# Performance work log

Measured on AMD Instinct MI355X. Metric: run time of the kernel, lower is better.

Reference implementation:

```python
import jax, jax.numpy as jnp
import numpy as np

B, T, N, F_IN = 8, 12, 20000, 2
H, HORIZON, K = 64, 12, 2
E = 320000


def setup_inputs() -> dict:
    key = jax.random.key(0)
    ks = jax.random.split(key, 12)
    s = 0.05
    return dict(
        x=jax.random.normal(ks[0], (B, T, N, F_IN), jnp.float32),
        edge_index=jax.random.randint(ks[1], (2, E), 0, N),
        edge_weight=jax.random.uniform(ks[2], (E,), jnp.float32),
        enc_w=jax.random.normal(ks[3], (F_IN, H), jnp.float32) * s,
        enc_b=jnp.zeros((H,), jnp.float32),
        node_emb=jax.random.normal(ks[4], (N, H), jnp.float32) * s,
        w_ih=jax.random.normal(ks[5], (3 * H, H), jnp.float32) * s,
        w_hh=jax.random.normal(ks[6], (3 * H, H), jnp.float32) * s,
        b_ih=jnp.zeros((3 * H,), jnp.float32),
        b_hh=jnp.zeros((3 * H,), jnp.float32),
        filt_w=jax.random.normal(ks[7], (H * (2 * K + 1), H), jnp.float32) * s,
        filt_b=jnp.zeros((H,), jnp.float32),
        dec_w=jax.random.normal(ks[8], (H, F_IN * HORIZON), jnp.float32) * s,
        dec_b=jnp.zeros((F_IN * HORIZON,), jnp.float32),
    )


def _gru_last(x_seq, w_ih, w_hh, b_ih, b_hh):
    # x_seq: [BN, T, H] -> last hidden state [BN, H] (torch GRU gate math)
    bn = x_seq.shape[0]
    h0 = jnp.zeros((bn, H), x_seq.dtype)
    # precompute input-side gates: [T, BN, 3H]
    xg = jnp.swapaxes(jnp.einsum('bth,gh->btg', x_seq, w_ih) + b_ih, 0, 1)

    def step(h, xg_t):
        hg = h @ w_hh.T + b_hh
        xr, xz, xn = jnp.split(xg_t, 3, axis=-1)
        hr, hz, hn = jnp.split(hg, 3, axis=-1)
        r = jax.nn.sigmoid(xr + hr)
        z = jax.nn.sigmoid(xz + hz)
        n = jnp.tanh(xn + r * hn)
        return (1.0 - z) * n + z * h, None

    h_last, _ = jax.lax.scan(step, h0, xg)
    return h_last


def _norm_weights(w, idx):
    # normalize edge weights by in-degree of aggregation index (tsl normalize)
    deg = jax.ops.segment_sum(w, idx, num_segments=N)
    inv = jnp.where(deg > 0, 1.0 / deg, 0.0)
    return w * inv[idx]


def _propagate(h, src, tgt, w):
    # h: [B, N, H]; message x_j * w aggregated (sum) at target
    msg = h[:, src, :] * w[None, :, None]           # [B, E, H]
    return jnp.zeros_like(h).at[:, tgt, :].add(msg)


def reference(x, edge_index, edge_weight, enc_w, enc_b, node_emb,
              w_ih, w_hh, b_ih, b_hh, filt_w, filt_b, dec_w, dec_b):
    b, t, n, _ = x.shape
    # linear encode + node embeddings
    x_emb = x @ enc_w + enc_b + node_emb[None, None]          # [B, T, N, H]
    # per-node GRU over time
    x_rnn = jnp.transpose(x_emb, (0, 2, 1, 3)).reshape(b * n, t, H)
    h = _gru_last(x_rnn, w_ih, w_hh, b_ih, b_hh).reshape(b, n, H)
    # diffusion graph conv: root + k hops forward + k hops backward
    src, tgt = edge_index[0], edge_index[1]
    w_fwd = _norm_weights(edge_weight, tgt)
    w_bwd = _norm_weights(edge_weight, src)
    outs = [h]
    for s_idx, t_idx, w in ((src, tgt, w_fwd), (tgt, src, w_bwd)):
        hs = h
        for _ in range(K):
            hs = _propagate(hs, s_idx, t_idx, w)
            outs.append(hs)
    z = jnp.concatenate(outs, axis=-1) @ filt_w + filt_b      # [B, N, H]
    # decode and rearrange 'b n (t f) -> b t n f'
    x_out = z @ dec_w + dec_b                                 # [B, N, HORIZON*F_IN]
    x_hor = x_out.reshape(b, n, HORIZON, F_IN)
    return jnp.transpose(x_hor, (0, 2, 1, 3))                 # [B, HORIZON, N, F_IN]
```

## Files before the change

kernel.cpp:

```cpp
#include <hip/hip_runtime.h>

#define NN 20000
#define NE 320000
#define NB 8
#define NT 12

typedef unsigned int u32;
typedef short bf16x8 __attribute__((ext_vector_type(8)));
typedef float f32x4 __attribute__((ext_vector_type(4)));
typedef u32   u32x2 __attribute__((ext_vector_type(2)));

union U8 { u32 u[4]; bf16x8 v; };

__device__ __forceinline__ float bcast(float v, int k) {
  return __int_as_float(__builtin_amdgcn_readlane(__float_as_int(v), k));
}
__device__ __forceinline__ u32 cvt_pk_bf16(float a, float b) {
  u32 r;
  asm("v_cvt_pk_bf16_f32 %0, %1, %2" : "=v"(r) : "v"(a), "v"(b));
  return r;
}
__device__ __forceinline__ float rcpf(float x) {
  float r;
  asm("v_rcp_f32 %0, %1" : "=v"(r) : "v"(x));
  return r;
}
__device__ __forceinline__ unsigned short f2bf(float f) {
  u32 u = __float_as_uint(f);
  u32 r = (u + 0x7FFFu + ((u >> 16) & 1u)) >> 16;
  return (unsigned short)r;
}
__device__ __forceinline__ float bf2f(unsigned short s) {
  return __uint_as_float(((u32)s) << 16);
}

__global__ void deg_kernel(const int* __restrict__ ei, const float* __restrict__ ew,
                           float* __restrict__ wsum_f, float* __restrict__ wsum_b,
                           int* __restrict__ cnt_f, int* __restrict__ cnt_b) {
  int e = blockIdx.x * 256 + threadIdx.x;
  if (e >= NE) return;
  int s = ei[e], t = ei[NE + e];
  float wv = ew[e];
  atomicAdd(&wsum_f[t], wv);
  atomicAdd(&cnt_f[t], 1);
  atomicAdd(&wsum_b[s], wv);
  atomicAdd(&cnt_b[s], 1);
}

__global__ __launch_bounds__(1024) void scan_kernel(
    const int* __restrict__ cnt_f, const int* __restrict__ cnt_b,
    int* __restrict__ rp_f, int* __restrict__ rp_b,
    int* __restrict__ cur_f, int* __restrict__ cur_b) {
  __shared__ int sm[1024];
  const int tid = threadIdx.x;
  for (int pass = 0; pass < 2; ++pass) {
    const int* cnt = pass ? cnt_b : cnt_f;
    int* rp  = pass ? rp_b  : rp_f;
    int* cur = pass ? cur_b : cur_f;
    const int base = tid * 20;
    int4 c4[5];
    int s = 0;
    if (base < NN) {
      const int4* cp = (const int4*)(cnt + base);
#pragma unroll
      for (int j = 0; j < 5; j++) c4[j] = cp[j];
#pragma unroll
      for (int j = 0; j < 5; j++) s += c4[j].x + c4[j].y + c4[j].z + c4[j].w;
    }
    __syncthreads();
    sm[tid] = s;
    __syncthreads();
    for (int off = 1; off < 1024; off <<= 1) {
      int v = (tid >= off) ? sm[tid - off] : 0;
      __syncthreads();
      sm[tid] += v;
      __syncthreads();
    }
    if (base < NN) {
      int run = sm[tid] - s;
      int4* rp4  = (int4*)(rp + base);
      int4* cur4 = (int4*)(cur + base);
#pragma unroll
      for (int j = 0; j < 5; j++) {
        int4 o;
        o.x = run; run += c4[j].x;
        o.y = run; run += c4[j].y;
        o.z = run; run += c4[j].z;
        o.w = run; run += c4[j].w;
        rp4[j] = o;
        cur4[j] = o;
      }
    }
    if (tid == 1023) rp[NN] = sm[1023];
  }
}

__global__ void fill_kernel(const int* __restrict__ ei, const float* __restrict__ ew,
                            const float* __restrict__ wsum_f, const float* __restrict__ wsum_b,
                            int* __restrict__ cur_f, int* __restrict__ cur_b,
                            int* __restrict__ col_f, float* __restrict__ wn_f,
                            int* __restrict__ col_b, float* __restrict__ wn_b) {
  int e = blockIdx.x * 256 + threadIdx.x;
  if (e >= NE) return;
  int s = ei[e], t = ei[NE + e];
  float wv = ew[e];
  int slot = atomicAdd(&cur_f[t], 1);
  float w1 = wsum_f[t];
  col_f[slot] = s;
  wn_f[slot] = (w1 > 0.f) ? wv / w1 : 0.f;
  slot = atomicAdd(&cur_b[s], 1);
  float w2 = wsum_b[s];
  col_b[slot] = t;
  wn_b[slot] = (w2 > 0.f) ? wv / w2 : 0.f;
}

#define NBLK_NB 313
__global__ __launch_bounds__(512) void nb_kernel(
    const float* __restrict__ node_emb, const float* __restrict__ enc_b,
    const float* __restrict__ w_ih, const float* __restrict__ b_ih,
    const float* __restrict__ enc_w, const float* __restrict__ b_hh,
    const float* __restrict__ filt_w, const float* __restrict__ filt_b,
    const float* __restrict__ dec_w, const float* __restrict__ dec_b,
    float* __restrict__ nbq, float* __restrict__ W2,
    float* __restrict__ Wcat, float* __restrict__ cbv) {
  const int tid = threadIdx.x;
  if (blockIdx.x >= NBLK_NB) {
    int idx = (blockIdx.x - NBLK_NB) * 512 + tid;
    if (idx < 64 * 128) {
      int k = idx >> 7, j = idx & 127;
      float acc = 0.f;
      if (j < 120) {
        int wi = j / 24, jj = j - wi * 24;
        for (int c = 0; c < 64; c++)
          acc += filt_w[(wi * 64 + k) * 64 + c] * dec_w[c * 24 + jj];
      }
      Wcat[idx] = acc;
    } else if (idx < 64 * 128 + 24) {
      int jj = idx - 64 * 128;
      float acc = dec_b[jj];
      for (int c = 0; c < 64; c++) acc += filt_b[c] * dec_w[c * 24 + jj];
      cbv[jj] = acc;
    }
    return;
  }
  __shared__ float w3[64 * 64 * 4];
  for (int idx = tid; idx < 192 * 64; idx += 512) {
    int row = idx >> 6, k = idx & 63;
    w3[((k << 6) + (row & 63)) * 4 + (row >> 6)] = w_ih[idx];
  }
  __syncthreads();
  const int lane = tid & 63, wave = tid >> 6;
  const float4* w3v = (const float4*)w3;
  const float eb = enc_b[lane];
  const float bir = b_ih[lane], biz = b_ih[64 + lane], bin_ = b_ih[128 + lane];
  const float bhr = b_hh[lane], bhz = b_hh[64 + lane];
#pragma unroll 1
  for (int pass = 0; pass < 8; ++pass) {
    const int n = blockIdx.x * 64 + pass * 8 + wave;
    if (n >= NN) break;
    float ne = node_emb[n * 64 + lane] + eb;
    float ar = bir, az = biz, an = bin_;
#pragma unroll 16
    for (int k = 0; k < 64; k++) {
      float4 w = w3v[(k << 6) + lane];
      float nk = bcast(ne, k);
      ar = fmaf(w.x, nk, ar);
      az = fmaf(w.y, nk, az);
      an = fmaf(w.z, nk, an);
    }
    nbq[(((lane >> 2)) * NN + n) * 4 + (lane & 3)]      = ar + bhr;
    nbq[((16 + (lane >> 2)) * NN + n) * 4 + (lane & 3)] = az + bhz;
    nbq[((32 + (lane >> 2)) * NN + n) * 4 + (lane & 3)] = an;
  }
  if (blockIdx.x == 0 && tid < 384) {
    int f = tid / 192, g = tid - f * 192;
    float acc = 0.f;
    for (int k2 = 0; k2 < 64; k2++) acc += enc_w[f * 64 + k2] * w_ih[g * 64 + k2];
    W2[f * 192 + g] = acc;
  }
}

#define MFMA(acc, a, b) acc = __builtin_amdgcn_mfma_f32_16x16x32_bf16((a), (b), acc, 0, 0, 0)

__global__ __launch_bounds__(256) void gru_kernel(
    const float* __restrict__ x, const float* __restrict__ nbq,
    const float* __restrict__ W2, const float* __restrict__ b_hh,
    const float* __restrict__ w_hh, const float* __restrict__ Wcat,
    const float* __restrict__ cbv,
    float* __restrict__ G0, float* __restrict__ G1f, float* __restrict__ G2f,
    float* __restrict__ G1b, float* __restrict__ G2b) {
  __shared__ u32 lds[16384];
  const int tid = threadIdx.x;

  for (int e = tid; e < 6144; e += 256) {
    int gate = e >> 5, k2 = (e & 31) << 1;
    float w0 = w_hh[gate * 64 + k2];
    float w1 = w_hh[gate * 64 + k2 + 1];
    unsigned short h0 = f2bf(w0), h1 = f2bf(w1);
    unsigned short l0 = f2bf(w0 - bf2f(h0)), l1 = f2bf(w1 - bf2f(h1));
    int tile = gate >> 4, ks = k2 >> 5;
    int ln = (gate & 15) + (((k2 >> 3) & 3) << 4);
    int r = (k2 >> 1) & 3;
    int idx = ((tile * 2 + ks) << 8) + (ln << 2) + r;
    lds[idx]        = (u32)h0 | ((u32)h1 << 16);
    lds[6144 + idx] = (u32)l0 | ((u32)l1 << 16);
  }
  __syncthreads();

  const int lane = tid & 63, wave = tid >> 6;
  const int g = lane >> 4, sl = lane & 15;
  const int seq = blockIdx.x * 64 + wave * 16 + sl;
  const int bb = seq / NN;
  const int node = seq - bb * NN;
  const u32 hxbase = 12288 + wave * 1024;
  const u32 xsw = ((u32)(sl & 3)) << 2;

  u32 w2h[12], w2l[12];
#pragma unroll
  for (int tl = 0; tl < 12; tl++) {
    float w0 = W2[tl * 16 + sl], w1 = W2[192 + tl * 16 + sl];
    u32 ph = cvt_pk_bf16(w0, w1);
    float lo0 = w0 - __uint_as_float(ph << 16);
    float lo1 = w1 - __uint_as_float(ph & 0xffff0000u);
    u32 pl = cvt_pk_bf16(lo0, lo1);
    w2h[tl] = (lane < 16) ? ph : 0u;
    w2l[tl] = (lane < 16) ? pl : 0u;
  }

  f32x4 nbA[4], nbB[4], nbC[4], bhnv[4];
#pragma unroll
  for (int fb = 0; fb < 4; fb++) {
    nbA[fb]  = *(const f32x4*)(nbq + ((size_t)(fb * 4 + g) * NN + node) * 4);
    nbB[fb]  = *(const f32x4*)(nbq + ((size_t)(16 + fb * 4 + g) * NN + node) * 4);
    nbC[fb]  = *(const f32x4*)(nbq + ((size_t)(32 + fb * 4 + g) * NN + node) * 4);
    bhnv[fb] = *(const f32x4*)(b_hh + 128 + fb * 16 + g * 4);
  }

  f32x4 hreg[4];
#pragma unroll
  for (int fb = 0; fb < 4; fb++) hreg[fb] = (f32x4){0.f, 0.f, 0.f, 0.f};

  const float* xptr = x + ((size_t)(bb * NT) * NN + node) * 2;

#define LDW(tile, ks, part) (*(const bf16x8*)(lds + (part) * 6144 + (((tile) * 2 + (ks)) << 8) + (lane << 2)))
#define RDX(q) (*(const bf16x8*)(lds + hxbase + (q) * 256 + sl * 16 + (((u32)(g * 4)) ^ xsw)))

  bf16x8 hb0, hb1, lb0, lb1;

  float2 xv = *(const float2*)(xptr);

#pragma unroll 1
  for (int t = 0; t < NT; t++) {
    float2 xvn;
    if (t + 1 < NT) xvn = *(const float2*)(xptr + (size_t)(t + 1) * (NN * 2));
    u32 xhw = cvt_pk_bf16(xv.x, xv.y);
    float xl0 = xv.x - __uint_as_float(xhw << 16);
    float xl1 = xv.y - __uint_as_float(xhw & 0xffff0000u);
    u32 xlw = cvt_pk_bf16(xl0, xl1);
    U8 xB;
    xB.u[0] = xhw; xB.u[1] = xlw; xB.u[2] = xhw; xB.u[3] = 0u;

    if (t) { hb0 = RDX(0); hb1 = RDX(1); lb0 = RDX(2); lb1 = RDX(3); }

#pragma unroll
    for (int fb = 0; fb < 4; fb++) {
      f32x4 aR = nbA[fb], aZ = nbB[fb], aXN = nbC[fb], aHN = bhnv[fb];
      if (t) {
        bf16x8 Ah0 = LDW(fb, 0, 0), Al0 = LDW(fb, 0, 1);
        bf16x8 Ah1 = LDW(fb, 1, 0), Al1 = LDW(fb, 1, 1);
        MFMA(aR, Ah0, hb0); MFMA(aR, Ah0, lb0); MFMA(aR, Al0, hb0);
        MFMA(aR, Ah1, hb1); MFMA(aR, Ah1, lb1); MFMA(aR, Al1, hb1);
        bf16x8 Bh0 = LDW(4 + fb, 0, 0), Bl0 = LDW(4 + fb, 0, 1);
        bf16x8 Bh1 = LDW(4 + fb, 1, 0), Bl1 = LDW(4 + fb, 1, 1);
        MFMA(aZ, Bh0, hb0); MFMA(aZ, Bh0, lb0); MFMA(aZ, Bl0, hb0);
        MFMA(aZ, Bh1, hb1); MFMA(aZ, Bh1, lb1); MFMA(aZ, Bl1, hb1);
        bf16x8 Ch0 = LDW(8 + fb, 0, 0), Cl0 = LDW(8 + fb, 0, 1);
        bf16x8 Ch1 = LDW(8 + fb, 1, 0), Cl1 = LDW(8 + fb, 1, 1);
        MFMA(aHN, Ch0, hb0); MFMA(aHN, Ch0, lb0); MFMA(aHN, Cl0, hb0);
        MFMA(aHN, Ch1, hb1); MFMA(aHN, Ch1, lb1); MFMA(aHN, Cl1, hb1);
      }
      U8 aW;
      aW.u[0] = w2h[fb];     aW.u[1] = w2h[fb];     aW.u[2] = w2l[fb];     aW.u[3] = 0u;
      MFMA(aR, aW.v, xB.v);
      aW.u[0] = w2h[4 + fb]; aW.u[1] = w2h[4 + fb]; aW.u[2] = w2l[4 + fb];
      MFMA(aZ, aW.v, xB.v);
      aW.u[0] = w2h[8 + fb]; aW.u[1] = w2h[8 + fb]; aW.u[2] = w2l[8 + fb];
      MFMA(aXN, aW.v, xB.v);

      float hv[4];
#pragma unroll
      for (int r = 0; r < 4; r++) {
        float rr = rcpf(1.f + __expf(-aR[r]));
        float zz = rcpf(1.f + __expf(-aZ[r]));
        float nv = fmaf(rr, aHN[r], aXN[r]);
        float th = fmaf(-2.f, rcpf(1.f + __expf(2.f * nv)), 1.f);
        float h2 = fmaf(zz, hreg[fb][r] - th, th);
        hreg[fb][r] = h2;
        hv[r] = h2;
      }
      u32 hiA = cvt_pk_bf16(hv[0], hv[1]);
      u32 hiB = cvt_pk_bf16(hv[2], hv[3]);
      float l0 = hv[0] - __uint_as_float(hiA << 16);
      float l1 = hv[1] - __uint_as_float(hiA & 0xffff0000u);
      float l2 = hv[2] - __uint_as_float(hiB << 16);
      float l3 = hv[3] - __uint_as_float(hiB & 0xffff0000u);
      u32 loA = cvt_pk_bf16(l0, l1);
      u32 loB = cvt_pk_bf16(l2, l3);
      u32 wo = hxbase + ((u32)(fb >> 1)) * 256 + sl * 16 + (((u32)((fb & 1) * 8 + g * 2)) ^ xsw);
      *(u32x2*)(lds + wo)       = (u32x2){hiA, hiB};
      *(u32x2*)(lds + wo + 512) = (u32x2){loA, loB};
    }
    xv = xvn;
  }

  __syncthreads();
  for (int e = tid; e < 4096; e += 256) {
    int j = e >> 5, k2 = (e & 31) << 1;
    float w0 = Wcat[k2 * 128 + j];
    float w1 = Wcat[(k2 + 1) * 128 + j];
    unsigned short h0 = f2bf(w0), h1 = f2bf(w1);
    unsigned short l0 = f2bf(w0 - bf2f(h0)), l1 = f2bf(w1 - bf2f(h1));
    int tile = j >> 4, ks = k2 >> 5;
    int ln = (j & 15) + (((k2 >> 3) & 3) << 4);
    int r = (k2 >> 1) & 3;
    int idx = ((tile * 2 + ks) << 8) + (ln << 2) + r;
    lds[idx]        = (u32)h0 | ((u32)h1 << 16);
    lds[4096 + idx] = (u32)l0 | ((u32)l1 << 16);
  }
  __syncthreads();
  hb0 = RDX(0); hb1 = RDX(1); lb0 = RDX(2); lb1 = RDX(3);

#define LDC(tile, ks, part) (*(const bf16x8*)(lds + (part) * 4096 + (((tile) * 2 + (ks)) << 8) + (lane << 2)))
#pragma unroll
  for (int tile = 0; tile < 8; tile++) {
    f32x4 acc = (f32x4){0.f, 0.f, 0.f, 0.f};
    bf16x8 Ah0 = LDC(tile, 0, 0), Al0 = LDC(tile, 0, 1);
    MFMA(acc, Ah0, hb0); MFMA(acc, Ah0, lb0); MFMA(acc, Al0, hb0);
    bf16x8 Ah1 = LDC(tile, 1, 0), Al1 = LDC(tile, 1, 1);
    MFMA(acc, Ah1, hb1); MFMA(acc, Ah1, lb1); MFMA(acc, Al1, hb1);
#pragma unroll
    for (int r = 0; r < 4; r++) {
      int j = tile * 16 + g * 4 + r;
      if (j < 120) {
        int wi = j / 24, jj = j - wi * 24;
        float val = acc[r];
        if (wi == 0) val += cbv[jj];
        float* gb = (wi == 0) ? G0 : (wi == 1) ? G1f : (wi == 2) ? G2f : (wi == 3) ? G1b : G2b;
        gb[((size_t)node * NB + bb) * 24 + jj] = val;
      }
    }
  }
}

__global__ __launch_bounds__(256) void hop1_kernel(
    float* __restrict__ G1f, const float* __restrict__ G2f,
    float* __restrict__ G1b, const float* __restrict__ G2b,
    const int* __restrict__ rp_f, const int* __restrict__ col_f, const float* __restrict__ wn_f,
    const int* __restrict__ rp_b, const int* __restrict__ col_b, const float* __restrict__ wn_b) {
  const int wv = threadIdx.x >> 6;
  const int lane = threadIdx.x & 63;
  const int task = blockIdx.x * 4 + wv;
  const int fwd = task < NN;
  const int n = fwd ? task : task - NN;
  const int* rp  = fwd ? rp_f : rp_b;
  const int* col = fwd ? col_f : col_b;
  const float* wn = fwd ? wn_f : wn_b;
  const float4* src = (const float4*)(fwd ? G2f : G2b);
  float4* dst = (float4*)(fwd ? G1f : G1b);
  const int e0 = rp[n], e1 = rp[n + 1];
  if (lane >= 48) return;
  float4 acc = {0.f, 0.f, 0.f, 0.f};
  for (int e = e0; e < e1; ++e) {
    const int c = col[e];
    const float w = wn[e];
    float4 v = src[(size_t)c * 48 + lane];
    acc.x = fmaf(w, v.x, acc.x);
    acc.y = fmaf(w, v.y, acc.y);
    acc.z = fmaf(w, v.z, acc.z);
    acc.w = fmaf(w, v.w, acc.w);
  }
  float4 d = dst[(size_t)n * 48 + lane];
  d.x += acc.x; d.y += acc.y; d.z += acc.z; d.w += acc.w;
  dst[(size_t)n * 48 + lane] = d;
}

__global__ __launch_bounds__(256) void hop2_kernel(
    float* __restrict__ G0, const float* __restrict__ G1f, const float* __restrict__ G1b,
    const int* __restrict__ rp_f, const int* __restrict__ col_f, const float* __restrict__ wn_f,
    const int* __restrict__ rp_b, const int* __restrict__ col_b, const float* __restrict__ wn_b) {
  const int wv = threadIdx.x >> 6;
  const int lane = threadIdx.x & 63;
  const int n = blockIdx.x * 4 + wv;
  if (lane >= 48) return;
  const float4* s1 = (const float4*)G1f;
  const float4* s2 = (const float4*)G1b;
  float4* dst = (float4*)G0;
  float4 acc = dst[(size_t)n * 48 + lane];
  int e0 = rp_f[n], e1 = rp_f[n + 1];
  for (int e = e0; e < e1; ++e) {
    const int c = col_f[e];
    const float w = wn_f[e];
    float4 v = s1[(size_t)c * 48 + lane];
    acc.x = fmaf(w, v.x, acc.x);
    acc.y = fmaf(w, v.y, acc.y);
    acc.z = fmaf(w, v.z, acc.z);
    acc.w = fmaf(w, v.w, acc.w);
  }
  e0 = rp_b[n]; e1 = rp_b[n + 1];
  for (int e = e0; e < e1; ++e) {
    const int c = col_b[e];
    const float w = wn_b[e];
    float4 v = s2[(size_t)c * 48 + lane];
    acc.x = fmaf(w, v.x, acc.x);
    acc.y = fmaf(w, v.y, acc.y);
    acc.z = fmaf(w, v.z, acc.z);
    acc.w = fmaf(w, v.w, acc.w);
  }
  dst[(size_t)n * 48 + lane] = acc;
}

__global__ __launch_bounds__(256) void reorder_kernel(const float* __restrict__ G0,
                                                      float* __restrict__ out) {
  __shared__ float tile[32 * 193];
  const int n0 = blockIdx.x * 32;
  const int tid = threadIdx.x;
  for (int idx = tid; idx < 6144; idx += 256) {
    int i = idx / 192, r = idx - i * 192;
    tile[i * 193 + r] = G0[(size_t)n0 * 192 + idx];
  }
  __syncthreads();
  for (int idx = tid; idx < 6144; idx += 256) {
    int b = idx / 768;
    int rem = idx - b * 768;
    int t = rem >> 6;
    int rem2 = rem & 63;
    int i = rem2 >> 1, f = rem2 & 1;
    out[(((size_t)b * NT + t) * NN + n0 + i) * 2 + f] = tile[i * 193 + b * 24 + t * 2 + f];
  }
}

extern "C" void kernel_launch(void* const* d_in, const int* in_sizes, int n_in,
                              void* d_out, int out_size, void* d_ws, size_t ws_size,
                              hipStream_t stream) {
  const float* x        = (const float*)d_in[0];
  const int*   ei       = (const int*)d_in[1];
  const float* ew       = (const float*)d_in[2];
  const float* enc_w    = (const float*)d_in[3];
  const float* enc_b    = (const float*)d_in[4];
  const float* node_emb = (const float*)d_in[5];
  const float* w_ih     = (const float*)d_in[6];
  const float* w_hh     = (const float*)d_in[7];
  const float* b_ih     = (const float*)d_in[8];
  const float* b_hh     = (const float*)d_in[9];
  const float* filt_w   = (const float*)d_in[10];
  const float* filt_b   = (const float*)d_in[11];
  const float* dec_w    = (const float*)d_in[12];
  const float* dec_b    = (const float*)d_in[13];
  float* out = (float*)d_out;

  char* p = (char*)d_ws;
  auto alloc = [&](size_t bytes) {
    char* r = p;
    p += (bytes + 255) & ~(size_t)255;
    return r;
  };
  const size_t BN24 = (size_t)NB * NN * 24;
  float* G0   = (float*)alloc(BN24 * 4);
  float* G1f  = (float*)alloc(BN24 * 4);
  float* G2f  = (float*)alloc(BN24 * 4);
  float* G1b  = (float*)alloc(BN24 * 4);
  float* G2b  = (float*)alloc(BN24 * 4);
  float* nbq  = (float*)alloc((size_t)NN * 192 * 4);
  int* rp_f   = (int*)alloc((NN + 1) * 4);
  int* rp_b   = (int*)alloc((NN + 1) * 4);
  char* zreg  = alloc(4 * NN * 4);
  float* wsum_f = (float*)zreg;
  float* wsum_b = wsum_f + NN;
  int*   cnt_f  = (int*)(wsum_b + NN);
  int*   cnt_b  = cnt_f + NN;
  int* cur_f  = (int*)alloc(NN * 4);
  int* cur_b  = (int*)alloc(NN * 4);
  int* col_f  = (int*)alloc((size_t)NE * 4);
  float* wn_f = (float*)alloc((size_t)NE * 4);
  int* col_b  = (int*)alloc((size_t)NE * 4);
  float* wn_b = (float*)alloc((size_t)NE * 4);
  float* Wcat = (float*)alloc(64 * 128 * 4);
  float* cbv  = (float*)alloc(32 * 4);
  float* W2   = (float*)alloc(384 * 4);

  hipMemsetAsync(zreg, 0, 4 * NN * 4, stream);
  deg_kernel<<<(NE + 255) / 256, 256, 0, stream>>>(ei, ew, wsum_f, wsum_b, cnt_f, cnt_b);
  scan_kernel<<<1, 1024, 0, stream>>>(cnt_f, cnt_b, rp_f, rp_b, cur_f, cur_b);
  fill_kernel<<<(NE + 255) / 256, 256, 0, stream>>>(ei, ew, wsum_f, wsum_b, cur_f, cur_b,
                                                    col_f, wn_f, col_b, wn_b);
  nb_kernel<<<NBLK_NB + 17, 512, 0, stream>>>(node_emb, enc_b, w_ih, b_ih, enc_w, b_hh,
                                              filt_w, filt_b, dec_w, dec_b,
                                              nbq, W2, Wcat, cbv);
  gru_kernel<<<(NB * NN) / 64, 256, 0, stream>>>(x, nbq, W2, b_hh, w_hh, Wcat, cbv,
                                                 G0, G1f, G2f, G1b, G2b);
  hop1_kernel<<<2 * NN / 4, 256, 0, stream>>>(G1f, G2f, G1b, G2b,
                                              rp_f, col_f, wn_f, rp_b, col_b, wn_b);
  hop2_kernel<<<NN / 4, 256, 0, stream>>>(G0, G1f, G1b,
                                          rp_f, col_f, wn_f, rp_b, col_b, wn_b);
  reorder_kernel<<<NN / 32, 256, 0, stream>>>(G0, out);
}
```

Measured before the change: 580.9 us.

## Cache recurrent GRU weight fragments in registers and relayout hidden-state LDS

Preloads the r-gate weight fragments (hi and lo) and the z-gate hi fragments from LDS into registers once before the time loop, so each step issues fewer LDS reads. It also changes the hidden-state LDS layout from an XOR-swizzled per-row scheme to a lane-contiguous layout matching the MFMA B-operand read pattern. A launch-bounds occupancy hint of 2 blocks per CU is added. The extra register arrays add pressure, and the hint may force spills. Removing the swizzle may introduce bank conflicts on the hidden-state writes.

```diff
diff --git a/kernel.cpp b/kernel.cpp
--- a/kernel.cpp
+++ b/kernel.cpp
@@ -182,7 +182,7 @@
 
 #define MFMA(acc, a, b) acc = __builtin_amdgcn_mfma_f32_16x16x32_bf16((a), (b), acc, 0, 0, 0)
 
-__global__ __launch_bounds__(256) void gru_kernel(
+__global__ __launch_bounds__(256, 2) void gru_kernel(
     const float* __restrict__ x, const float* __restrict__ nbq,
     const float* __restrict__ W2, const float* __restrict__ b_hh,
     const float* __restrict__ w_hh, const float* __restrict__ Wcat,
@@ -213,7 +213,19 @@
   const int bb = seq / NN;
   const int node = seq - bb * NN;
   const u32 hxbase = 12288 + wave * 1024;
-  const u32 xsw = ((u32)(sl & 3)) << 2;
+
+#define LDW(tile, ks, part) (*(const bf16x8*)(lds + (part) * 6144 + (((tile) * 2 + (ks)) << 8) + (lane << 2)))
+#define RDX(q) (*(const bf16x8*)(lds + hxbase + (q) * 256 + (lane << 2)))
+
+  bf16x8 rA[4][2][2];
+  bf16x8 zA[4][2];
+#pragma unroll
+  for (int fb = 0; fb < 4; fb++) {
+    rA[fb][0][0] = LDW(fb, 0, 0); rA[fb][0][1] = LDW(fb, 0, 1);
+    rA[fb][1][0] = LDW(fb, 1, 0); rA[fb][1][1] = LDW(fb, 1, 1);
+    zA[fb][0] = LDW(4 + fb, 0, 0);
+    zA[fb][1] = LDW(4 + fb, 1, 0);
+  }
 
   u32 w2h[12], w2l[12];
 #pragma unroll
@@ -241,9 +253,6 @@
   for (int fb = 0; fb < 4; fb++) hreg[fb] = (f32x4){0.f, 0.f, 0.f, 0.f};
 
   const float* xptr = x + ((size_t)(bb * NT) * NN + node) * 2;
-
-#define LDW(tile, ks, part) (*(const bf16x8*)(lds + (part) * 6144 + (((tile) * 2 + (ks)) << 8) + (lane << 2)))
-#define RDX(q) (*(const bf16x8*)(lds + hxbase + (q) * 256 + sl * 16 + (((u32)(g * 4)) ^ xsw)))
 
   bf16x8 hb0, hb1, lb0, lb1;
 
@@ -266,14 +275,11 @@
     for (int fb = 0; fb < 4; fb++) {
       f32x4 aR = nbA[fb], aZ = nbB[fb], aXN = nbC[fb], aHN = bhnv[fb];
       if (t) {
-        bf16x8 Ah0 = LDW(fb, 0, 0), Al0 = LDW(fb, 0, 1);
-        bf16x8 Ah1 = LDW(fb, 1, 0), Al1 = LDW(fb, 1, 1);
-        MFMA(aR, Ah0, hb0); MFMA(aR, Ah0, lb0); MFMA(aR, Al0, hb0);
-        MFMA(aR, Ah1, hb1); MFMA(aR, Ah1, lb1); MFMA(aR, Al1, hb1);
-        bf16x8 Bh0 = LDW(4 + fb, 0, 0), Bl0 = LDW(4 + fb, 0, 1);
-        bf16x8 Bh1 = LDW(4 + fb, 1, 0), Bl1 = LDW(4 + fb, 1, 1);
-        MFMA(aZ, Bh0, hb0); MFMA(aZ, Bh0, lb0); MFMA(aZ, Bl0, hb0);
-        MFMA(aZ, Bh1, hb1); MFMA(aZ, Bh1, lb1); MFMA(aZ, Bl1, hb1);
+        MFMA(aR, rA[fb][0][0], hb0); MFMA(aR, rA[fb][0][0], lb0); MFMA(aR, rA[fb][0][1], hb0);
+        MFMA(aR, rA[fb][1][0], hb1); MFMA(aR, rA[fb][1][0], lb1); MFMA(aR, rA[fb][1][1], hb1);
+        bf16x8 Bl0 = LDW(4 + fb, 0, 1), Bl1 = LDW(4 + fb, 1, 1);
+        MFMA(aZ, zA[fb][0], hb0); MFMA(aZ, zA[fb][0], lb0); MFMA(aZ, Bl0, hb0);
+        MFMA(aZ, zA[fb][1], hb1); MFMA(aZ, zA[fb][1], lb1); MFMA(aZ, Bl1, hb1);
         bf16x8 Ch0 = LDW(8 + fb, 0, 0), Cl0 = LDW(8 + fb, 0, 1);
         bf16x8 Ch1 = LDW(8 + fb, 1, 0), Cl1 = LDW(8 + fb, 1, 1);
         MFMA(aHN, Ch0, hb0); MFMA(aHN, Ch0, lb0); MFMA(aHN, Cl0, hb0);
@@ -306,7 +312,8 @@
       float l3 = hv[3] - __uint_as_float(hiB & 0xffff0000u);
       u32 loA = cvt_pk_bf16(l0, l1);
       u32 loB = cvt_pk_bf16(l2, l3);
-      u32 wo = hxbase + ((u32)(fb >> 1)) * 256 + sl * 16 + (((u32)((fb & 1) * 8 + g * 2)) ^ xsw);
+      u32 wo = hxbase + ((u32)(fb >> 1)) * 256
+             + ((u32)((fb & 1) * 2 + (g >> 1))) * 64 + (u32)(sl * 4) + (u32)((g & 1) * 2);
       *(u32x2*)(lds + wo)       = (u32x2){hiA, hiB};
       *(u32x2*)(lds + wo + 512) = (u32x2){loA, loB};
     }
```

Result: slower. 619.3 us (+6.6%).
